# Kernel tuning notes

Measured on AMD Instinct MI355X. Metric: run time of the kernel, lower is better.

Reference implementation:

```python
import jax, jax.numpy as jnp
import numpy as np

# Two atom types (e.g. H and O) with per-atom auxiliary basis dims 16 and 48.
N_H, D_H = 40000, 16   # number of H-type atoms, basis functions per H atom
N_O, D_O = 20000, 48   # number of O-type atoms, basis functions per O atom
C = 32                 # channels
EPS = 1e-6


def _psd(key, d):
    # Stand-in for the pyscf per-atom overlap matrix: symmetric PSD.
    a = jax.random.normal(key, (d, d), dtype=jnp.float32)
    return a @ a.T / d + 0.5 * jnp.eye(d, dtype=jnp.float32)


def setup_inputs() -> dict:
    key = jax.random.key(0)
    k1, k2, k3 = jax.random.split(key, 3)
    n_total = N_H * D_H + N_O * D_O  # 1,600,000 basis rows
    x = jax.random.normal(k1, (n_total, C), dtype=jnp.float32)
    S_H = _psd(k2, D_H)
    S_O = _psd(k3, D_O)
    # Index arrays equivalent to the boolean atomic_number_masks: all basis
    # functions of H-type atoms first, then O-type (contiguous per atom).
    idx_H = jnp.arange(N_H * D_H, dtype=jnp.int32)
    idx_O = jnp.arange(N_O * D_O, dtype=jnp.int32) + N_H * D_H
    return {"x": x, "S_H": S_H, "S_O": S_O, "idx_H": idx_H, "idx_O": idx_O}


def _l2_function_norm_atom(y, S):
    # y: [n_atoms, d, C], S: [d, d]
    # norm_{a,c} = sum_{i,j} S_ij * y_{a,i,c} * y_{a,j,c}
    norm = jnp.einsum('ij,aic,ajc->ac', S, y, y)
    norm = jnp.sqrt(norm)[:, None, :]  # [n_atoms, 1, C], matches unsqueeze(1)
    return y / (norm + EPS)


def reference(x, S_H, S_O, idx_H, idx_O):
    # H-type atoms: gather -> per-atom bilinear L2 norm -> scatter back
    y = x[idx_H].reshape(N_H, D_H, C)
    x = x.at[idx_H].set(_l2_function_norm_atom(y, S_H).reshape(-1, C))
    # O-type atoms (reads the updated x, as in the sequential torch loop;
    # index sets are disjoint so order does not change the result)
    y = x[idx_O].reshape(N_O, D_O, C)
    x = x.at[idx_O].set(_l2_function_norm_atom(y, S_O).reshape(-1, C))
    return x
```

## Files before the change

### kernel.cpp

```cpp
#include <hip/hip_runtime.h>
#include <cstdint>
#include <cstddef>

#define NH 40000
#define DH 16
#define NO 20000
#define DO_ 48
#define CH 32

typedef float f32x2 __attribute__((ext_vector_type(2)));

#define XO_BASE ((size_t)NH * DH * CH)
#define OBLOCKS (NO / 8)
#define HBLOCKS (NH / 16)

__global__ __launch_bounds__(256, 4) void l2norm_fused(
    const float* __restrict__ x, float* __restrict__ out,
    const float* __restrict__ SH, const float* __restrict__ SO) {
  const int b = blockIdx.x;
  const int idx = b >> 1;

  if ((b & 1) == 0) {
    const int c  = threadIdx.x & 31;
    const int al = threadIdx.x >> 5;
    const int atom = idx * 8 + al;
    const size_t base = XO_BASE + (size_t)atom * DO_ * CH + (size_t)c;

    float yv[DO_];
#pragma unroll
    for (int i = 0; i < DO_; ++i) yv[i] = x[base + (size_t)i * CH];
#pragma unroll
    for (int i = 0; i < DO_; ++i) asm volatile("" : "+v"(yv[i]));

    float acc = 0.f;
#pragma unroll
    for (int i = 0; i < DO_; ++i) {
      float s = 0.f;
#pragma unroll
      for (int j = 0; j < i; ++j)
        s = fmaf(SO[i * DO_ + j], yv[j], s);
      acc = fmaf(fmaf(SO[i * DO_ + i], yv[i], 2.f * s), yv[i], acc);
    }

    const float inv = 1.f / (sqrtf(acc) + 1e-6f);
#pragma unroll
    for (int i = 0; i < DO_; ++i)
      __builtin_nontemporal_store(yv[i] * inv, (float*)&out[base + (size_t)i * CH]);
  } else {
    const f32x2* __restrict__ x2 = (const f32x2*)x;
    f32x2* __restrict__ o2 = (f32x2*)out;
    const int cp = threadIdx.x & 15;
    const int al = threadIdx.x >> 4;
    const int atom = idx * 16 + al;
    const size_t base = (size_t)atom * DH * 16 + (size_t)cp;

    f32x2 yv[DH];
#pragma unroll
    for (int i = 0; i < DH; ++i) yv[i] = x2[base + (size_t)i * 16];
#pragma unroll
    for (int i = 0; i < DH; ++i) asm volatile("" : "+v"(yv[i]));

    float ax = 0.f, ay = 0.f;
#pragma unroll
    for (int i = 0; i < DH; ++i) {
      float sx = 0.f, sy = 0.f;
#pragma unroll
      for (int j = 0; j < i; ++j) {
        const float s = SH[i * DH + j];
        sx = fmaf(s, yv[j].x, sx);
        sy = fmaf(s, yv[j].y, sy);
      }
      const float sd = SH[i * DH + i];
      ax = fmaf(fmaf(sd, yv[i].x, 2.f * sx), yv[i].x, ax);
      ay = fmaf(fmaf(sd, yv[i].y, 2.f * sy), yv[i].y, ay);
    }

    const float ix = 1.f / (sqrtf(ax) + 1e-6f);
    const float iy = 1.f / (sqrtf(ay) + 1e-6f);
#pragma unroll
    for (int i = 0; i < DH; ++i) {
      f32x2 r;
      r.x = yv[i].x * ix;
      r.y = yv[i].y * iy;
      __builtin_nontemporal_store(r, &o2[base + (size_t)i * 16]);
    }
  }
}

extern "C" void kernel_launch(void* const* d_in, const int* in_sizes, int n_in,
                              void* d_out, int out_size, void* d_ws, size_t ws_size,
                              hipStream_t stream) {
  const float* x  = (const float*)d_in[0];
  const float* SH = (const float*)d_in[1];
  const float* SO = (const float*)d_in[2];
  float* out = (float*)d_out;

  l2norm_fused<<<OBLOCKS + HBLOCKS, 256, 0, stream>>>(x, out, SH, SO);
}
```

Measured before the change: 349.2 us.

## Tile O-atom bilinear form into 8-row blocks with float2 channels, re-reading x

The O-type path now gives each thread two channels as float2 and 16 atoms per block. It evaluates the 48x48 quadratic form in 8x8 tiles, reloading y tiles from global memory instead of holding all 48 values in registers, and re-reads x for the final scaled write. This is meant to cut register pressure and raise occupancy. The block interleave changes to 1 O block per 2 H blocks, and launch-bounds occupancy hints, asm register pins and nontemporal stores are dropped. The cost is extra global or cache reads of x per O atom.

```diff
diff --git a/kernel.cpp b/kernel.cpp
--- a/kernel.cpp
+++ b/kernel.cpp
@@ -10,55 +10,84 @@
 
 typedef float f32x2 __attribute__((ext_vector_type(2)));
 
-#define XO_BASE ((size_t)NH * DH * CH)
-#define OBLOCKS (NO / 8)
+#define XO_BASE2 ((size_t)NH * DH * CH / 2)
+#define OBLOCKS (NO / 16)
 #define HBLOCKS (NH / 16)
 
-__global__ __launch_bounds__(256, 4) void l2norm_fused(
-    const float* __restrict__ x, float* __restrict__ out,
+__global__ __launch_bounds__(256) void l2norm_fused(
+    const f32x2* __restrict__ x2, f32x2* __restrict__ o2,
     const float* __restrict__ SH, const float* __restrict__ SO) {
   const int b = blockIdx.x;
-  const int idx = b >> 1;
+  const int cp = threadIdx.x & 15;
+  const int al = threadIdx.x >> 4;
 
-  if ((b & 1) == 0) {
-    const int c  = threadIdx.x & 31;
-    const int al = threadIdx.x >> 5;
-    const int atom = idx * 8 + al;
-    const size_t base = XO_BASE + (size_t)atom * DO_ * CH + (size_t)c;
+  if (b % 3 == 0) {
+    const int atom = (b / 3) * 16 + al;
+    const size_t base = XO_BASE2 + (size_t)atom * (DO_ * CH / 2) + (size_t)cp;
 
-    float yv[DO_];
+    float ax = 0.f, ay = 0.f;
+    f32x2 yi[8], yj[8];
 #pragma unroll
-    for (int i = 0; i < DO_; ++i) yv[i] = x[base + (size_t)i * CH];
+    for (int ti = 0; ti < 6; ++ti) {
 #pragma unroll
-    for (int i = 0; i < DO_; ++i) asm volatile("" : "+v"(yv[i]));
-
-    float acc = 0.f;
+      for (int k = 0; k < 8; ++k)
+        yi[k] = x2[base + (size_t)(ti * 8 + k) * 16];
 #pragma unroll
-    for (int i = 0; i < DO_; ++i) {
-      float s = 0.f;
+      for (int i = 0; i < 8; ++i) {
+        float sx = 0.f, sy = 0.f;
 #pragma unroll
-      for (int j = 0; j < i; ++j)
-        s = fmaf(SO[i * DO_ + j], yv[j], s);
-      acc = fmaf(fmaf(SO[i * DO_ + i], yv[i], 2.f * s), yv[i], acc);
+        for (int j = 0; j < i; ++j) {
+          const float s = SO[(ti * 8 + i) * DO_ + ti * 8 + j];
+          sx = fmaf(s, yi[j].x, sx);
+          sy = fmaf(s, yi[j].y, sy);
+        }
+        const float sd = SO[(ti * 8 + i) * DO_ + ti * 8 + i];
+        ax = fmaf(fmaf(sd, yi[i].x, 2.f * sx), yi[i].x, ax);
+        ay = fmaf(fmaf(sd, yi[i].y, 2.f * sy), yi[i].y, ay);
+      }
+#pragma unroll
+      for (int tj = 0; tj < ti; ++tj) {
+#pragma unroll
+        for (int k = 0; k < 8; ++k)
+          yj[k] = x2[base + (size_t)(tj * 8 + k) * 16];
+#pragma unroll
+        for (int i = 0; i < 8; ++i) {
+          float sx = 0.f, sy = 0.f;
+#pragma unroll
+          for (int j = 0; j < 8; ++j) {
+            const float s = SO[(ti * 8 + i) * DO_ + tj * 8 + j];
+            sx = fmaf(s, yj[j].x, sx);
+            sy = fmaf(s, yj[j].y, sy);
+          }
+          ax = fmaf(2.f * sx, yi[i].x, ax);
+          ay = fmaf(2.f * sy, yi[i].y, ay);
+        }
+      }
     }
 
-    const float inv = 1.f / (sqrtf(acc) + 1e-6f);
+    const float ix = 1.f / (sqrtf(ax) + 1e-6f);
+    const float iy = 1.f / (sqrtf(ay) + 1e-6f);
 #pragma unroll
-    for (int i = 0; i < DO_; ++i)
-      __builtin_nontemporal_store(yv[i] * inv, (float*)&out[base + (size_t)i * CH]);
+    for (int t = 0; t < 6; ++t) {
+#pragma unroll
+      for (int k = 0; k < 8; ++k)
+        yi[k] = x2[base + (size_t)(t * 8 + k) * 16];
+#pragma unroll
+      for (int k = 0; k < 8; ++k) {
+        f32x2 r;
+        r.x = yi[k].x * ix;
+        r.y = yi[k].y * iy;
+        o2[base + (size_t)(t * 8 + k) * 16] = r;
+      }
+    }
   } else {
-    const f32x2* __restrict__ x2 = (const f32x2*)x;
-    f32x2* __restrict__ o2 = (f32x2*)out;
-    const int cp = threadIdx.x & 15;
-    const int al = threadIdx.x >> 4;
-    const int atom = idx * 16 + al;
-    const size_t base = (size_t)atom * DH * 16 + (size_t)cp;
+    const int hidx = (b / 3) * 2 + (b % 3) - 1;
+    const int atom = hidx * 16 + al;
+    const size_t base = (size_t)atom * (DH * CH / 2) + (size_t)cp;
 
     f32x2 yv[DH];
 #pragma unroll
     for (int i = 0; i < DH; ++i) yv[i] = x2[base + (size_t)i * 16];
-#pragma unroll
-    for (int i = 0; i < DH; ++i) asm volatile("" : "+v"(yv[i]));
 
     float ax = 0.f, ay = 0.f;
 #pragma unroll
@@ -82,7 +111,7 @@
       f32x2 r;
       r.x = yv[i].x * ix;
       r.y = yv[i].y * iy;
-      __builtin_nontemporal_store(r, &o2[base + (size_t)i * 16]);
+      o2[base + (size_t)i * 16] = r;
     }
   }
 }
@@ -95,5 +124,6 @@
   const float* SO = (const float*)d_in[2];
   float* out = (float*)d_out;
 
-  l2norm_fused<<<OBLOCKS + HBLOCKS, 256, 0, stream>>>(x, out, SH, SO);
+  l2norm_fused<<<OBLOCKS + HBLOCKS, 256, 0, stream>>>(
+      (const f32x2*)x, (f32x2*)out, SH, SO);
 }
```

Result: slower. 377.4 us (+8.1%).

## Split O-atom bilinear norm across a wavefront using LDS-staged S and shuffles

Applied to the files above, without the earlier changes.

O-type atoms are now processed by a full 64-lane wavefront per atom: S_O is staged in shared memory, each lane holds 12 rows of two channels, and a row-blocked matrix-vector product is computed via cross-lane shuffles followed by a shuffle reduction. This cuts per-thread register pressure and serial FMA chains, at the cost of dropping the symmetric half-product trick and adding LDS and shuffle traffic. Block interleaving changes to two O blocks per H block, nontemporal stores become regular stores, and the occupancy hint is removed.

```diff
diff --git a/kernel.cpp b/kernel.cpp
--- a/kernel.cpp
+++ b/kernel.cpp
@@ -9,56 +9,94 @@
 #define CH 32
 
 typedef float f32x2 __attribute__((ext_vector_type(2)));
+typedef float f32x4 __attribute__((ext_vector_type(4)));
 
-#define XO_BASE ((size_t)NH * DH * CH)
-#define OBLOCKS (NO / 8)
+#define XO_BASE2 ((size_t)NH * DH * CH / 2)
+#define OBLOCKS (NO / 4)
 #define HBLOCKS (NH / 16)
 
-__global__ __launch_bounds__(256, 4) void l2norm_fused(
-    const float* __restrict__ x, float* __restrict__ out,
+__global__ __launch_bounds__(256) void l2norm_fused(
+    const f32x2* __restrict__ x2, f32x2* __restrict__ o2,
     const float* __restrict__ SH, const float* __restrict__ SO) {
+  __shared__ __align__(16) float S_lds[DO_ * DO_];
   const int b = blockIdx.x;
-  const int idx = b >> 1;
+  const int t = threadIdx.x;
 
-  if ((b & 1) == 0) {
-    const int c  = threadIdx.x & 31;
-    const int al = threadIdx.x >> 5;
-    const int atom = idx * 8 + al;
-    const size_t base = XO_BASE + (size_t)atom * DO_ * CH + (size_t)c;
+  if (b % 3 != 2) {
+    const int oidx = (b / 3) * 2 + (b % 3);
+#pragma unroll
+    for (int k = 0; k < 9; ++k) S_lds[k * 256 + t] = SO[k * 256 + t];
+    __syncthreads();
 
-    float yv[DO_];
+    const int lane = t & 63;
+    const int q = lane >> 4;
+    const int cp = lane & 15;
+    const int atom = oidx * 4 + (t >> 6);
+    const size_t base = XO_BASE2 + (size_t)atom * (DO_ * CH / 2);
+
+    f32x2 yr[12];
 #pragma unroll
-    for (int i = 0; i < DO_; ++i) yv[i] = x[base + (size_t)i * CH];
+    for (int m = 0; m < 12; ++m)
+      yr[m] = x2[base + (size_t)(4 * m + q) * 16 + cp];
+
+    f32x2 z[12];
 #pragma unroll
-    for (int i = 0; i < DO_; ++i) asm volatile("" : "+v"(yv[i]));
+    for (int m = 0; m < 12; ++m) z[m] = f32x2{0.f, 0.f};
 
-    float acc = 0.f;
+    const float* Sq = &S_lds[q * DO_];
+
 #pragma unroll
-    for (int i = 0; i < DO_; ++i) {
-      float s = 0.f;
+    for (int ms = 0; ms < 12; ++ms) {
+      float bx[4], by[4];
 #pragma unroll
-      for (int j = 0; j < i; ++j)
-        s = fmaf(SO[i * DO_ + j], yv[j], s);
-      acc = fmaf(fmaf(SO[i * DO_ + i], yv[i], 2.f * s), yv[i], acc);
+      for (int di = 0; di < 4; ++di) {
+        bx[di] = __shfl(yr[ms].x, di * 16 + cp, 64);
+        by[di] = __shfl(yr[ms].y, di * 16 + cp, 64);
+      }
+#pragma unroll
+      for (int mp = 0; mp < 12; ++mp) {
+        const f32x4 s4 = *(const f32x4*)&Sq[(4 * mp) * DO_ + 4 * ms];
+        z[mp].x = fmaf(s4.x, bx[0], z[mp].x);
+        z[mp].y = fmaf(s4.x, by[0], z[mp].y);
+        z[mp].x = fmaf(s4.y, bx[1], z[mp].x);
+        z[mp].y = fmaf(s4.y, by[1], z[mp].y);
+        z[mp].x = fmaf(s4.z, bx[2], z[mp].x);
+        z[mp].y = fmaf(s4.z, by[2], z[mp].y);
+        z[mp].x = fmaf(s4.w, bx[3], z[mp].x);
+        z[mp].y = fmaf(s4.w, by[3], z[mp].y);
+      }
     }
 
-    const float inv = 1.f / (sqrtf(acc) + 1e-6f);
+    float nx = 0.f, ny = 0.f;
 #pragma unroll
-    for (int i = 0; i < DO_; ++i)
-      __builtin_nontemporal_store(yv[i] * inv, (float*)&out[base + (size_t)i * CH]);
+    for (int m = 0; m < 12; ++m) {
+      nx = fmaf(yr[m].x, z[m].x, nx);
+      ny = fmaf(yr[m].y, z[m].y, ny);
+    }
+    nx += __shfl_xor(nx, 16, 64);
+    nx += __shfl_xor(nx, 32, 64);
+    ny += __shfl_xor(ny, 16, 64);
+    ny += __shfl_xor(ny, 32, 64);
+
+    const float ix = 1.f / (sqrtf(nx) + 1e-6f);
+    const float iy = 1.f / (sqrtf(ny) + 1e-6f);
+#pragma unroll
+    for (int m = 0; m < 12; ++m) {
+      f32x2 r;
+      r.x = yr[m].x * ix;
+      r.y = yr[m].y * iy;
+      o2[base + (size_t)(4 * m + q) * 16 + cp] = r;
+    }
   } else {
-    const f32x2* __restrict__ x2 = (const f32x2*)x;
-    f32x2* __restrict__ o2 = (f32x2*)out;
-    const int cp = threadIdx.x & 15;
-    const int al = threadIdx.x >> 4;
-    const int atom = idx * 16 + al;
-    const size_t base = (size_t)atom * DH * 16 + (size_t)cp;
+    const int hidx = b / 3;
+    const int cp = t & 15;
+    const int al = t >> 4;
+    const int atom = hidx * 16 + al;
+    const size_t base = (size_t)atom * (DH * CH / 2) + (size_t)cp;
 
     f32x2 yv[DH];
 #pragma unroll
     for (int i = 0; i < DH; ++i) yv[i] = x2[base + (size_t)i * 16];
-#pragma unroll
-    for (int i = 0; i < DH; ++i) asm volatile("" : "+v"(yv[i]));
 
     float ax = 0.f, ay = 0.f;
 #pragma unroll
@@ -82,7 +120,7 @@
       f32x2 r;
       r.x = yv[i].x * ix;
       r.y = yv[i].y * iy;
-      __builtin_nontemporal_store(r, &o2[base + (size_t)i * 16]);
+      o2[base + (size_t)i * 16] = r;
     }
   }
 }
@@ -95,5 +133,6 @@
   const float* SO = (const float*)d_in[2];
   float* out = (float*)d_out;
 
-  l2norm_fused<<<OBLOCKS + HBLOCKS, 256, 0, stream>>>(x, out, SH, SO);
+  l2norm_fused<<<OBLOCKS + HBLOCKS, 256, 0, stream>>>(
+      (const f32x2*)x, (f32x2*)out, SH, SO);
 }
```

Result: no change. 344.7 us (-1.3%).
